# Kernel tuning notes

Hardware: AMD Instinct MI355X
Metric: run time of the kernel (lower is better)

Reference implementation:

```python
import jax, jax.numpy as jnp
import numpy as np

INPUT_SIZE = 256
HIDDEN_SIZE = 1024
N_MODULES = 8
BATCH = 64
SEQ_LEN = 2048


def setup_inputs() -> dict:
    key = jax.random.key(0)
    ks = jax.random.split(key, 7)
    H, I = HIDDEN_SIZE, INPUT_SIZE
    return {
        "x": jax.random.normal(ks[0], (BATCH, SEQ_LEN, I), dtype=jnp.float32),
        "weight_ih": jax.random.normal(ks[1], (H, I), dtype=jnp.float32) * 0.02,
        "weight_hh": jax.random.normal(ks[2], (H, H), dtype=jnp.float32) * 0.02,
        "bias_ih": jax.random.normal(ks[3], (H,), dtype=jnp.float32) * 0.02,
        "bias_hh": jax.random.normal(ks[4], (H,), dtype=jnp.float32) * 0.02,
        "fc_w": jax.random.normal(ks[5], (I, H), dtype=jnp.float32) * 0.02,
        "fc_b": jax.random.normal(ks[6], (I,), dtype=jnp.float32) * 0.02,
        "n_modules": N_MODULES,
    }


def reference(x, weight_ih, weight_hh, bias_ih, bias_hh, fc_w, fc_b, n_modules):
    b, T, _ = x.shape
    H = weight_hh.shape[0]
    ms = H // n_modules  # module_size
    # Block-triangular mask: row block i of weight_hh only sees hidden cols >= i*ms
    rows = jnp.arange(H)[:, None]
    cols = jnp.arange(H)[None, :]
    tri = (cols >= (rows // ms) * ms).astype(weight_hh.dtype)  # [H, H]
    Whh = weight_hh * tri
    periods = 2 ** jnp.arange(n_modules)  # [M] clockwork periods

    def step(h, inp):
        xt, t = inp  # xt: [b, I], t: scalar time index
        active = (t % periods) == 0                      # [M]
        amask = jnp.repeat(active, ms)                   # [H]
        cand = jnp.tanh(xt @ weight_ih.T + bias_ih + h @ Whh.T + bias_hh)  # [b, H]
        h_new = jnp.where(amask[None, :], cand, h)
        y = h_new @ fc_w.T + fc_b                        # [b, I]
        return h_new, y

    h0 = jnp.zeros((b, H), dtype=x.dtype)
    xs = jnp.swapaxes(x, 0, 1)  # [T, b, I]
    _, ys = jax.lax.scan(step, h0, (xs, jnp.arange(T)))
    return jnp.swapaxes(ys, 0, 1)  # [b, T, I]
```

## Files before the change

### kernel.cpp

```cpp
#include <hip/hip_runtime.h>
#include <cstdio>

typedef __attribute__((ext_vector_type(8))) short bf16x8;
typedef __attribute__((ext_vector_type(4))) float f32x4;

__device__ inline unsigned short f2bf(float f) {
  unsigned u = __builtin_bit_cast(unsigned, f);
  u += 0x7fffu + ((u >> 16) & 1u);
  return (unsigned short)(u >> 16);
}

struct PackArgs {
  const float* wih; const float* whh; const float* fcw;
  unsigned short* wp[8]; unsigned short* fcp;
};

__global__ __launch_bounds__(256) void pack_kernel(PackArgs a) {
  int id = blockIdx.x * 256 + threadIdx.x;
  int ph = blockIdx.y;
  if (ph == 8) {
    if (id < 256 * 1024) a.fcp[id] = f2bf(a.fcw[id]);
    return;
  }
  int Ktot = 256 + 128 * (7 - ph);
  if (id >= 128 * Ktot) return;
  int n = id / Ktot;
  int kc = id - n * Ktot;
  int row = ph * 128 + n;
  float v;
  if (kc < 256) {
    v = a.wih[row * 256 + kc];
  } else {
    int j = ph + 1 + ((kc - 256) >> 7);
    int c = (kc - 256) & 127;
    v = a.whh[row * 1024 + j * 128 + c];
  }
  a.wp[ph][id] = f2bf(v);
}

__global__ __launch_bounds__(256) void xconv_kernel(const float* __restrict__ x,
                                                    unsigned short* __restrict__ xb) {
  size_t i = ((size_t)blockIdx.x * 256 + threadIdx.x) * 8;
  f32x4 v0 = *(const f32x4*)(x + i);
  f32x4 v1 = *(const f32x4*)(x + i + 4);
  bf16x8 o;
  o[0] = (short)f2bf(v0[0]); o[1] = (short)f2bf(v0[1]);
  o[2] = (short)f2bf(v0[2]); o[3] = (short)f2bf(v0[3]);
  o[4] = (short)f2bf(v1[0]); o[5] = (short)f2bf(v1[1]);
  o[6] = (short)f2bf(v1[2]); o[7] = (short)f2bf(v1[3]);
  *(bf16x8*)(xb + i) = o;
}

struct GArgs {
  const float* x;
  const unsigned short* xb;
  const unsigned short* hs[8];
  int hShift[8];
  int hK[8];
  int nH;
  const unsigned short* Wp;
  int Ktot;
  const float* bias1;
  const float* bias2;
  int biasOff;
  float* out;
  int Kcnt, kShift, tOff, kLog, kMask, useX, xbf;
};

template <int N, int WM, int MREP>
__global__ __launch_bounds__(256) void egemm(GArgs g) {
  constexpr int WN = 4 / WM;
  constexpr int NT = N / (16 * WN);
  const int tid = threadIdx.x;
  const int lane = tid & 63;
  const int w = tid >> 6;
  const int mw = (WM == 1) ? 0 : (w & 1);
  const int nw = (WM == 1) ? w : (w >> 1);
  const int l15 = lane & 15, l4 = lane >> 4;
  const int waveRow0 = blockIdx.x * (WM * MREP * 16) + mw * (MREP * 16);
  const int colBase = nw * (NT * 16);

  int bA[MREP], kA[MREP];
#pragma unroll
  for (int i = 0; i < MREP; ++i) {
    int r = waveRow0 + i * 16 + l15;
    bA[i] = r >> g.kLog;
    kA[i] = r & g.kMask;
  }

  f32x4 acc[MREP][NT];
#pragma unroll
  for (int i = 0; i < MREP; ++i)
#pragma unroll
    for (int nt = 0; nt < NT; ++nt) acc[i][nt] = (f32x4){0.f, 0.f, 0.f, 0.f};

  int kglob = 0;
  if (g.useX) {
    if (g.xbf) {
      const unsigned short* xr[MREP];
#pragma unroll
      for (int i = 0; i < MREP; ++i)
        xr[i] = g.xb + ((size_t)bA[i] * 2048 + ((size_t)kA[i] << g.kShift)) * 256 + l4 * 8;
#pragma unroll
      for (int kt = 0; kt < 256; kt += 32) {
        bf16x8 bfrag[NT];
#pragma unroll
        for (int nt = 0; nt < NT; ++nt)
          bfrag[nt] = *(const bf16x8*)(g.Wp + (size_t)(colBase + nt * 16 + l15) * g.Ktot + kt + l4 * 8);
#pragma unroll
        for (int i = 0; i < MREP; ++i) {
          bf16x8 af = *(const bf16x8*)(xr[i] + kt);
#pragma unroll
          for (int nt = 0; nt < NT; ++nt)
            acc[i][nt] = __builtin_amdgcn_mfma_f32_16x16x32_bf16(af, bfrag[nt], acc[i][nt], 0, 0, 0);
        }
      }
    } else {
      const float* xr[MREP];
#pragma unroll
      for (int i = 0; i < MREP; ++i)
        xr[i] = g.x + ((size_t)bA[i] * 2048 + ((size_t)kA[i] << g.kShift)) * 256 + l4 * 8;
#pragma unroll
      for (int kt = 0; kt < 256; kt += 32) {
        bf16x8 bfrag[NT];
#pragma unroll
        for (int nt = 0; nt < NT; ++nt)
          bfrag[nt] = *(const bf16x8*)(g.Wp + (size_t)(colBase + nt * 16 + l15) * g.Ktot + kt + l4 * 8);
#pragma unroll
        for (int i = 0; i < MREP; ++i) {
          f32x4 x0 = *(const f32x4*)(xr[i] + kt);
          f32x4 x1 = *(const f32x4*)(xr[i] + kt + 4);
          bf16x8 af;
          af[0] = (short)f2bf(x0[0]); af[1] = (short)f2bf(x0[1]);
          af[2] = (short)f2bf(x0[2]); af[3] = (short)f2bf(x0[3]);
          af[4] = (short)f2bf(x1[0]); af[5] = (short)f2bf(x1[1]);
          af[6] = (short)f2bf(x1[2]); af[7] = (short)f2bf(x1[3]);
#pragma unroll
          for (int nt = 0; nt < NT; ++nt)
            acc[i][nt] = __builtin_amdgcn_mfma_f32_16x16x32_bf16(af, bfrag[nt], acc[i][nt], 0, 0, 0);
        }
      }
    }
    kglob = 256;
  }

  for (int s = 0; s < g.nH; ++s) {
    const unsigned short* rp[MREP];
    int valid[MREP];
#pragma unroll
    for (int i = 0; i < MREP; ++i) {
      int t = (kA[i] << g.kShift) + g.tOff;
      valid[i] = (t >= 0);
      int idx = (valid[i] ? t : 0) >> g.hShift[s];
      rp[i] = g.hs[s] + (((size_t)(bA[i] * g.hK[s] + idx)) << 7) + l4 * 8;
    }
#pragma unroll
    for (int kt = 0; kt < 128; kt += 32) {
      bf16x8 bfrag[NT];
#pragma unroll
      for (int nt = 0; nt < NT; ++nt)
        bfrag[nt] = *(const bf16x8*)(g.Wp + (size_t)(colBase + nt * 16 + l15) * g.Ktot + kglob + kt + l4 * 8);
#pragma unroll
      for (int i = 0; i < MREP; ++i) {
        bf16x8 af = *(const bf16x8*)(rp[i] + kt);
        if (!valid[i]) {
#pragma unroll
          for (int e = 0; e < 8; ++e) af[e] = 0;
        }
#pragma unroll
        for (int nt = 0; nt < NT; ++nt)
          acc[i][nt] = __builtin_amdgcn_mfma_f32_16x16x32_bf16(af, bfrag[nt], acc[i][nt], 0, 0, 0);
      }
    }
    kglob += 128;
  }

#pragma unroll
  for (int nt = 0; nt < NT; ++nt) {
    int col = colBase + nt * 16 + l15;
    float bias = g.bias1[g.biasOff + col];
    if (g.bias2) bias += g.bias2[g.biasOff + col];
#pragma unroll
    for (int i = 0; i < MREP; ++i) {
#pragma unroll
      for (int q = 0; q < 4; ++q) {
        int gr = waveRow0 + i * 16 + l4 * 4 + q;
        g.out[(size_t)gr * N + col] = acc[i][nt][q] + bias;
      }
    }
  }
}

__global__ __launch_bounds__(512) void recur_kernel(
    const float* __restrict__ whh, const float* __restrict__ E,
    unsigned short* __restrict__ Hm, int m, int Kcnt, int L, int W) {
  const int c = blockIdx.x, b = blockIdx.y;
  const int tid = threadIdx.x;
  const int r = tid >> 2, q = tid & 3;
  const int kBeg = c * L;
  const int kEnd = min(kBeg + L, Kcnt);
  const int ws = max(0, kBeg - W);

  float A[32];
  const float* arow = whh + (size_t)(m * 128 + r) * 1024 + m * 128 + q * 32;
#pragma unroll
  for (int cc = 0; cc < 32; cc += 4) *(f32x4*)&A[cc] = *(const f32x4*)(arow + cc);

  __shared__ float hb[2][144];
  if (tid < 128) hb[0][tid + ((tid >> 5) << 2)] = 0.f;
  __syncthreads();

  const float* Eb = E + (size_t)b * Kcnt * 128;
  unsigned short* Hb = Hm + (size_t)b * Kcnt * 128;
  const int wr = r + ((r >> 5) << 2);
  float e0 = (q == 0) ? Eb[(size_t)ws * 128 + r] : 0.f;
  float e1 = (q == 0 && ws + 1 < kEnd) ? Eb[(size_t)(ws + 1) * 128 + r] : 0.f;

  int cur = 0;
  for (int k = ws; k < kEnd; ++k) {
    float ev = e0;
    e0 = e1;
    if (q == 0 && k + 2 < kEnd) e1 = Eb[(size_t)(k + 2) * 128 + r];
    const float* hv = &hb[cur][q * 36];
    float a0 = 0.f, a1 = 0.f, a2 = 0.f, a3 = 0.f;
#pragma unroll
    for (int cc = 0; cc < 32; cc += 4) {
      f32x4 h4 = *(const f32x4*)(hv + cc);
      a0 = fmaf(A[cc + 0], h4[0], a0);
      a1 = fmaf(A[cc + 1], h4[1], a1);
      a2 = fmaf(A[cc + 2], h4[2], a2);
      a3 = fmaf(A[cc + 3], h4[3], a3);
    }
    float acc = ((a0 + a1) + (a2 + a3)) + ev;
    acc += __shfl_xor(acc, 1, 64);
    acc += __shfl_xor(acc, 2, 64);
    if (q == 0) {
      float xc = fminf(fmaxf(acc, -30.f), 30.f);
      float ex = __expf(2.f * xc);
      float val = (ex - 1.f) / (ex + 1.f);
      hb[cur ^ 1][wr] = val;
      if (k >= kBeg) Hb[(size_t)k * 128 + r] = f2bf(val);
    }
    asm volatile("s_waitcnt lgkmcnt(0)" ::: "memory");
    __builtin_amdgcn_sched_barrier(0);
    __builtin_amdgcn_s_barrier();
    __builtin_amdgcn_sched_barrier(0);
    cur ^= 1;
  }
}

extern "C" void kernel_launch(void* const* d_in, const int* in_sizes, int n_in,
                              void* d_out, int out_size, void* d_ws, size_t ws_size,
                              hipStream_t stream) {
  const float* x   = (const float*)d_in[0];
  const float* wih = (const float*)d_in[1];
  const float* whh = (const float*)d_in[2];
  const float* bih = (const float*)d_in[3];
  const float* bhh = (const float*)d_in[4];
  const float* fcw = (const float*)d_in[5];
  const float* fcb = (const float*)d_in[6];

  char* p = (char*)d_ws;
  float* E = (float*)p; p += (size_t)64 * 2048 * 128 * 4;
  unsigned short* H[8];
  for (int m = 0; m < 8; ++m) { H[m] = (unsigned short*)p; p += (size_t)64 * (2048 >> m) * 128 * 2; }
  unsigned short* Wp[8];
  for (int m = 0; m < 8; ++m) { int Kt = 256 + 128 * (7 - m); Wp[m] = (unsigned short*)p; p += (size_t)128 * Kt * 2; }
  unsigned short* fcp = (unsigned short*)p; p += (size_t)256 * 1024 * 2;
  size_t need = (size_t)(p - (char*)d_ws);
  if (need > ws_size) {
    fprintf(stderr, "kernel_launch: ws too small: need %zu have %zu\n", need, ws_size);
    return;
  }
  unsigned short* xb = (unsigned short*)p;
  size_t needXb = need + (size_t)64 * 2048 * 256 * 2;
  int useXb = (needXb <= ws_size) ? 1 : 0;

  PackArgs pa;
  pa.wih = wih; pa.whh = whh; pa.fcw = fcw; pa.fcp = fcp;
  for (int m = 0; m < 8; ++m) pa.wp[m] = Wp[m];
  pack_kernel<<<dim3(1024, 9), 256, 0, stream>>>(pa);
  if (useXb) xconv_kernel<<<dim3(16384), 256, 0, stream>>>(x, xb);

  for (int m = 7; m >= 0; --m) {
    int Kcnt = 2048 >> m;
    GArgs a{};
    a.x = x; a.xb = xb; a.xbf = useXb; a.useX = 1;
    a.nH = 7 - m;
    for (int s = 0; s < a.nH; ++s) {
      int j = m + 1 + s;
      a.hs[s] = H[j]; a.hShift[s] = j; a.hK[s] = 2048 >> j;
    }
    a.Wp = Wp[m]; a.Ktot = 256 + 128 * (7 - m);
    a.bias1 = bih; a.bias2 = bhh; a.biasOff = m * 128;
    a.out = E; a.Kcnt = Kcnt; a.kShift = m; a.tOff = -1;
    a.kLog = 11 - m; a.kMask = Kcnt - 1;
    egemm<128, 2, 4><<<dim3(64 * Kcnt / 128), 256, 0, stream>>>(a);

    int L, W = 32;
    if (m == 0) L = 128;
    else if (m == 1) L = 64;
    else if (m <= 4) L = 32;
    else L = Kcnt;
    int nC = (Kcnt + L - 1) / L;
    recur_kernel<<<dim3(nC, 64), 512, 0, stream>>>(whh, E, H[m], m, Kcnt, L, W);
  }

  {
    GArgs a{};
    a.x = nullptr; a.xb = nullptr; a.xbf = 0; a.useX = 0; a.nH = 8;
    for (int j = 0; j < 8; ++j) { a.hs[j] = H[j]; a.hShift[j] = j; a.hK[j] = 2048 >> j; }
    a.Wp = fcp; a.Ktot = 1024;
    a.bias1 = fcb; a.bias2 = nullptr; a.biasOff = 0;
    a.out = (float*)d_out; a.Kcnt = 2048; a.kShift = 0; a.tOff = 0;
    a.kLog = 11; a.kMask = 2047;
    egemm<256, 1, 4><<<dim3(2048), 256, 0, stream>>>(a);
  }
}
```

Before: 1.154 ms.

## Stage GEMM operands through double-buffered LDS with direct global-to-LDS loads

Replaces the register-direct egemm template with egemm2, which stages 128x32 A and B tiles into double-buffered shared memory using global_load_lds and prefetches the next K slice while MFMAs run on the current one. Invalid (t<0) rows read from a zeroed workspace buffer instead of being masked in registers. The final FC GEMM is split into a 2D grid of 128x128 tiles. The aim is to improve operand reuse across waves and hide global load latency, at the cost of a barrier per K step and a vmcnt(0) wait that may serialize the loads.

```diff
diff --git a/kernel.cpp b/kernel.cpp
--- a/kernel.cpp
+++ b/kernel.cpp
@@ -1,5 +1,6 @@
 #include <hip/hip_runtime.h>
 #include <cstdio>
+#include <cstdint>
 
 typedef __attribute__((ext_vector_type(8))) short bf16x8;
 typedef __attribute__((ext_vector_type(4))) float f32x4;
@@ -10,14 +11,21 @@
   return (unsigned short)(u >> 16);
 }
 
+__device__ inline void gload16(const void* g, void* l) {
+  __builtin_amdgcn_global_load_lds(
+      (const __attribute__((address_space(1))) void*)g,
+      (__attribute__((address_space(3))) void*)l, 16, 0, 0);
+}
+
 struct PackArgs {
   const float* wih; const float* whh; const float* fcw;
-  unsigned short* wp[8]; unsigned short* fcp;
+  unsigned short* wp[8]; unsigned short* fcp; float* zbuf;
 };
 
 __global__ __launch_bounds__(256) void pack_kernel(PackArgs a) {
   int id = blockIdx.x * 256 + threadIdx.x;
   int ph = blockIdx.y;
+  if (ph == 9) { if (id < 1024) a.zbuf[id] = 0.f; return; }
   if (ph == 8) {
     if (id < 256 * 1024) a.fcp[id] = f2bf(a.fcw[id]);
     return;
@@ -64,130 +72,127 @@
   const float* bias2;
   int biasOff;
   float* out;
-  int Kcnt, kShift, tOff, kLog, kMask, useX, xbf;
+  const float* zbuf;
+  int ldOut, kShift, tOff, kLog, kMask, useX, xbf;
 };
 
-template <int N, int WM, int MREP>
-__global__ __launch_bounds__(256) void egemm(GArgs g) {
-  constexpr int WN = 4 / WM;
-  constexpr int NT = N / (16 * WN);
+__global__ __launch_bounds__(256) void egemm2(GArgs g) {
   const int tid = threadIdx.x;
   const int lane = tid & 63;
   const int w = tid >> 6;
-  const int mw = (WM == 1) ? 0 : (w & 1);
-  const int nw = (WM == 1) ? w : (w >> 1);
+  const int mw = w & 1, nw = w >> 1;
   const int l15 = lane & 15, l4 = lane >> 4;
-  const int waveRow0 = blockIdx.x * (WM * MREP * 16) + mw * (MREP * 16);
-  const int colBase = nw * (NT * 16);
-
-  int bA[MREP], kA[MREP];
-#pragma unroll
-  for (int i = 0; i < MREP; ++i) {
-    int r = waveRow0 + i * 16 + l15;
-    bA[i] = r >> g.kLog;
-    kA[i] = r & g.kMask;
-  }
-
-  f32x4 acc[MREP][NT];
-#pragma unroll
-  for (int i = 0; i < MREP; ++i)
-#pragma unroll
-    for (int nt = 0; nt < NT; ++nt) acc[i][nt] = (f32x4){0.f, 0.f, 0.f, 0.f};
-
-  int kglob = 0;
-  if (g.useX) {
-    if (g.xbf) {
-      const unsigned short* xr[MREP];
-#pragma unroll
-      for (int i = 0; i < MREP; ++i)
-        xr[i] = g.xb + ((size_t)bA[i] * 2048 + ((size_t)kA[i] << g.kShift)) * 256 + l4 * 8;
-#pragma unroll
-      for (int kt = 0; kt < 256; kt += 32) {
-        bf16x8 bfrag[NT];
-#pragma unroll
-        for (int nt = 0; nt < NT; ++nt)
-          bfrag[nt] = *(const bf16x8*)(g.Wp + (size_t)(colBase + nt * 16 + l15) * g.Ktot + kt + l4 * 8);
-#pragma unroll
-        for (int i = 0; i < MREP; ++i) {
-          bf16x8 af = *(const bf16x8*)(xr[i] + kt);
-#pragma unroll
-          for (int nt = 0; nt < NT; ++nt)
-            acc[i][nt] = __builtin_amdgcn_mfma_f32_16x16x32_bf16(af, bfrag[nt], acc[i][nt], 0, 0, 0);
-        }
+  const int blockRow0 = blockIdx.x * 128;
+  const int colBlk = blockIdx.y * 128;
+  const int xoff = g.useX ? 256 : 0;
+
+  __shared__ __align__(16) char smem[2][16384];
+
+  const int myH = w & 1;
+  const int ko0 = w >> 1;
+  const int rS = blockRow0 + myH * 64 + lane;
+  const int bS = rS >> g.kLog;
+  const int kS = rS & g.kMask;
+  const int tS = (kS << g.kShift) + g.tOff;
+  const int vS = tS >= 0;
+  const int tSc = vS ? tS : 0;
+  const char* xrowS = (const char*)(g.xb + ((size_t)bS * 2048 + ((size_t)kS << g.kShift)) * 256);
+  const char* bsrcRow = (const char*)(g.Wp + (size_t)(colBlk + myH * 64 + lane) * g.Ktot);
+
+  auto STAGE = [&](int sbuf, int tt) {
+    int kg = tt << 5;
+    bool xseg = g.useX && (kg < 256);
+    char* lb = &smem[sbuf][0];
+    if (!xseg || g.xbf) {
+      const char* asrc; int ktl;
+      if (xseg) { asrc = xrowS; ktl = kg; }
+      else {
+        int s = (kg - xoff) >> 7;
+        ktl = (kg - xoff) & 127;
+        asrc = vS ? (const char*)g.hs[s] +
+                        ((size_t)((size_t)bS * g.hK[s] + (tSc >> g.hShift[s])) << 8)
+                  : (const char*)g.zbuf;
       }
+      gload16(asrc + (size_t)(ktl + ko0 * 8) * 2, lb + ko0 * 2048 + myH * 1024);
+      gload16(asrc + (size_t)(ktl + (ko0 + 2) * 8) * 2, lb + (ko0 + 2) * 2048 + myH * 1024);
+    }
+    const char* bsrc = bsrcRow + (size_t)kg * 2;
+    char* lbB = lb + 8192;
+    gload16(bsrc + ko0 * 16, lbB + ko0 * 2048 + myH * 1024);
+    gload16(bsrc + (ko0 + 2) * 16, lbB + (ko0 + 2) * 2048 + myH * 1024);
+  };
+
+  const float* xF[4];
+  if (g.useX && !g.xbf) {
+#pragma unroll
+    for (int i = 0; i < 4; ++i) {
+      int r = blockRow0 + mw * 64 + i * 16 + l15;
+      int b = r >> g.kLog, k = r & g.kMask;
+      xF[i] = g.x + ((size_t)b * 2048 + ((size_t)k << g.kShift)) * 256 + l4 * 8;
+    }
+  }
+
+  f32x4 acc[4][4];
+#pragma unroll
+  for (int i = 0; i < 4; ++i)
+#pragma unroll
+    for (int nt = 0; nt < 4; ++nt) acc[i][nt] = (f32x4){0.f, 0.f, 0.f, 0.f};
+
+  const int NT32 = g.Ktot >> 5;
+  STAGE(0, 0);
+  asm volatile("s_waitcnt vmcnt(0)" ::: "memory");
+  __builtin_amdgcn_s_barrier();
+  __builtin_amdgcn_sched_barrier(0);
+
+  int buf = 0;
+  for (int t = 0; t < NT32; ++t) {
+    if (t + 1 < NT32) STAGE(buf ^ 1, t + 1);
+    int kg = t << 5;
+    const char* sb = &smem[buf][0];
+    bf16x8 bfr[4];
+#pragma unroll
+    for (int nt = 0; nt < 4; ++nt)
+      bfr[nt] = *(const bf16x8*)(sb + 8192 + l4 * 2048 + (nw * 64 + nt * 16 + l15) * 16);
+    bf16x8 afr[4];
+    bool aLds = g.xbf || !g.useX || (kg >= 256);
+    if (aLds) {
+#pragma unroll
+      for (int i = 0; i < 4; ++i)
+        afr[i] = *(const bf16x8*)(sb + l4 * 2048 + (mw * 64 + i * 16 + l15) * 16);
     } else {
-      const float* xr[MREP];
-#pragma unroll
-      for (int i = 0; i < MREP; ++i)
-        xr[i] = g.x + ((size_t)bA[i] * 2048 + ((size_t)kA[i] << g.kShift)) * 256 + l4 * 8;
-#pragma unroll
-      for (int kt = 0; kt < 256; kt += 32) {
-        bf16x8 bfrag[NT];
-#pragma unroll
-        for (int nt = 0; nt < NT; ++nt)
-          bfrag[nt] = *(const bf16x8*)(g.Wp + (size_t)(colBase + nt * 16 + l15) * g.Ktot + kt + l4 * 8);
-#pragma unroll
-        for (int i = 0; i < MREP; ++i) {
-          f32x4 x0 = *(const f32x4*)(xr[i] + kt);
-          f32x4 x1 = *(const f32x4*)(xr[i] + kt + 4);
-          bf16x8 af;
-          af[0] = (short)f2bf(x0[0]); af[1] = (short)f2bf(x0[1]);
-          af[2] = (short)f2bf(x0[2]); af[3] = (short)f2bf(x0[3]);
-          af[4] = (short)f2bf(x1[0]); af[5] = (short)f2bf(x1[1]);
-          af[6] = (short)f2bf(x1[2]); af[7] = (short)f2bf(x1[3]);
-#pragma unroll
-          for (int nt = 0; nt < NT; ++nt)
-            acc[i][nt] = __builtin_amdgcn_mfma_f32_16x16x32_bf16(af, bfrag[nt], acc[i][nt], 0, 0, 0);
-        }
+#pragma unroll
+      for (int i = 0; i < 4; ++i) {
+        f32x4 x0 = *(const f32x4*)(xF[i] + kg);
+        f32x4 x1 = *(const f32x4*)(xF[i] + kg + 4);
+        afr[i][0] = (short)f2bf(x0[0]); afr[i][1] = (short)f2bf(x0[1]);
+        afr[i][2] = (short)f2bf(x0[2]); afr[i][3] = (short)f2bf(x0[3]);
+        afr[i][4] = (short)f2bf(x1[0]); afr[i][5] = (short)f2bf(x1[1]);
+        afr[i][6] = (short)f2bf(x1[2]); afr[i][7] = (short)f2bf(x1[3]);
       }
     }
-    kglob = 256;
-  }
-
-  for (int s = 0; s < g.nH; ++s) {
-    const unsigned short* rp[MREP];
-    int valid[MREP];
-#pragma unroll
-    for (int i = 0; i < MREP; ++i) {
-      int t = (kA[i] << g.kShift) + g.tOff;
-      valid[i] = (t >= 0);
-      int idx = (valid[i] ? t : 0) >> g.hShift[s];
-      rp[i] = g.hs[s] + (((size_t)(bA[i] * g.hK[s] + idx)) << 7) + l4 * 8;
-    }
-#pragma unroll
-    for (int kt = 0; kt < 128; kt += 32) {
-      bf16x8 bfrag[NT];
-#pragma unroll
-      for (int nt = 0; nt < NT; ++nt)
-        bfrag[nt] = *(const bf16x8*)(g.Wp + (size_t)(colBase + nt * 16 + l15) * g.Ktot + kglob + kt + l4 * 8);
-#pragma unroll
-      for (int i = 0; i < MREP; ++i) {
-        bf16x8 af = *(const bf16x8*)(rp[i] + kt);
-        if (!valid[i]) {
-#pragma unroll
-          for (int e = 0; e < 8; ++e) af[e] = 0;
-        }
-#pragma unroll
-        for (int nt = 0; nt < NT; ++nt)
-          acc[i][nt] = __builtin_amdgcn_mfma_f32_16x16x32_bf16(af, bfrag[nt], acc[i][nt], 0, 0, 0);
+#pragma unroll
+    for (int i = 0; i < 4; ++i)
+#pragma unroll
+      for (int nt = 0; nt < 4; ++nt)
+        acc[i][nt] = __builtin_amdgcn_mfma_f32_16x16x32_bf16(afr[i], bfr[nt], acc[i][nt], 0, 0, 0);
+    asm volatile("s_waitcnt vmcnt(0)" ::: "memory");
+    __builtin_amdgcn_s_barrier();
+    __builtin_amdgcn_sched_barrier(0);
+    buf ^= 1;
+  }
+
+#pragma unroll
+  for (int nt = 0; nt < 4; ++nt) {
+    int colG = colBlk + nw * 64 + nt * 16 + l15;
+    float bias = g.bias1[g.biasOff + colG];
+    if (g.bias2) bias += g.bias2[g.biasOff + colG];
+#pragma unroll
+    for (int i = 0; i < 4; ++i)
+#pragma unroll
+      for (int q = 0; q < 4; ++q) {
+        int gr = blockRow0 + mw * 64 + i * 16 + l4 * 4 + q;
+        g.out[(size_t)gr * g.ldOut + colG] = acc[i][nt][q] + bias;
       }
-    }
-    kglob += 128;
-  }
-
-#pragma unroll
-  for (int nt = 0; nt < NT; ++nt) {
-    int col = colBase + nt * 16 + l15;
-    float bias = g.bias1[g.biasOff + col];
-    if (g.bias2) bias += g.bias2[g.biasOff + col];
-#pragma unroll
-    for (int i = 0; i < MREP; ++i) {
-#pragma unroll
-      for (int q = 0; q < 4; ++q) {
-        int gr = waveRow0 + i * 16 + l4 * 4 + q;
-        g.out[(size_t)gr * N + col] = acc[i][nt][q] + bias;
-      }
-    }
   }
 }
 
@@ -261,6 +266,7 @@
   const float* fcb = (const float*)d_in[6];
 
   char* p = (char*)d_ws;
+  float* zbuf = (float*)p; p += 4096;
   float* E = (float*)p; p += (size_t)64 * 2048 * 128 * 4;
   unsigned short* H[8];
   for (int m = 0; m < 8; ++m) { H[m] = (unsigned short*)p; p += (size_t)64 * (2048 >> m) * 128 * 2; }
@@ -273,13 +279,12 @@
     return;
   }
   unsigned short* xb = (unsigned short*)p;
-  size_t needXb = need + (size_t)64 * 2048 * 256 * 2;
-  int useXb = (needXb <= ws_size) ? 1 : 0;
+  int useXb = (need + (size_t)64 * 2048 * 256 * 2 <= ws_size) ? 1 : 0;
 
   PackArgs pa;
-  pa.wih = wih; pa.whh = whh; pa.fcw = fcw; pa.fcp = fcp;
+  pa.wih = wih; pa.whh = whh; pa.fcw = fcw; pa.fcp = fcp; pa.zbuf = zbuf;
   for (int m = 0; m < 8; ++m) pa.wp[m] = Wp[m];
-  pack_kernel<<<dim3(1024, 9), 256, 0, stream>>>(pa);
+  pack_kernel<<<dim3(1024, 10), 256, 0, stream>>>(pa);
   if (useXb) xconv_kernel<<<dim3(16384), 256, 0, stream>>>(x, xb);
 
   for (int m = 7; m >= 0; --m) {
@@ -293,9 +298,9 @@
     }
     a.Wp = Wp[m]; a.Ktot = 256 + 128 * (7 - m);
     a.bias1 = bih; a.bias2 = bhh; a.biasOff = m * 128;
-    a.out = E; a.Kcnt = Kcnt; a.kShift = m; a.tOff = -1;
-    a.kLog = 11 - m; a.kMask = Kcnt - 1;
-    egemm<128, 2, 4><<<dim3(64 * Kcnt / 128), 256, 0, stream>>>(a);
+    a.out = E; a.zbuf = zbuf; a.ldOut = 128;
+    a.kShift = m; a.tOff = -1; a.kLog = 11 - m; a.kMask = Kcnt - 1;
+    egemm2<<<dim3(64 * Kcnt / 128, 1), 256, 0, stream>>>(a);
 
     int L, W = 32;
     if (m == 0) L = 128;
@@ -312,8 +317,8 @@
     for (int j = 0; j < 8; ++j) { a.hs[j] = H[j]; a.hShift[j] = j; a.hK[j] = 2048 >> j; }
     a.Wp = fcp; a.Ktot = 1024;
     a.bias1 = fcb; a.bias2 = nullptr; a.biasOff = 0;
-    a.out = (float*)d_out; a.Kcnt = 2048; a.kShift = 0; a.tOff = 0;
-    a.kLog = 11; a.kMask = 2047;
-    egemm<256, 1, 4><<<dim3(2048), 256, 0, stream>>>(a);
-  }
-}
+    a.out = (float*)d_out; a.zbuf = zbuf; a.ldOut = 256;
+    a.kShift = 0; a.tOff = 0; a.kLog = 11; a.kMask = 2047;
+    egemm2<<<dim3(1024, 2), 256, 0, stream>>>(a);
+  }
+}
```

After: 1.004 ms. 1.15x faster.
